# Optimization experiments

Measured on AMD Instinct MI355X. Metric: run time of the kernel, lower is better.

## Reference

```python
import jax, jax.numpy as jnp
import numpy as np


def _rel_shift(x):
    # x: [qlen, klen, bsz, n_head]
    q, k, b, n = x.shape
    zero_pad = jnp.zeros((q, 1, b, n), dtype=x.dtype)
    x_padded = jnp.concatenate([zero_pad, x], axis=1)      # [q, k+1, b, n]
    x_padded = x_padded.reshape(k + 1, q, b, n)            # row-major view
    return x_padded[1:].reshape(q, k, b, n)


def setup_inputs() -> dict:
    key = jax.random.key(0)
    k1, k2, k3, k4, k5 = jax.random.split(key, 5)
    QLEN, KLEN, BSZ, NH, DH = 1024, 1024, 4, 16, 64
    return {
        "w_head_q": jax.random.normal(k1, (QLEN, BSZ, NH, DH), dtype=jnp.float32),
        "w_head_k": jax.random.normal(k2, (KLEN, BSZ, NH, DH), dtype=jnp.float32),
        "r_emb": jax.random.normal(k3, (KLEN, NH, DH), dtype=jnp.float32),
        "r_w_bias": jax.random.normal(k4, (NH, DH), dtype=jnp.float32),
        "r_bias": jax.random.normal(k5, (KLEN, NH), dtype=jnp.float32),
    }


def reference(w_head_q, w_head_k, r_emb, r_w_bias, r_bias):
    klen = w_head_k.shape[0]
    # klen <= r_emb.shape[0] branch: take the last klen relative positions
    r_emb = r_emb[-klen:]
    r_bias = r_bias[-klen:]

    rw_head_q = w_head_q + r_w_bias[None]                  # [q, b, n, d]
    AC = jnp.einsum('ibnd,jbnd->ijbn', rw_head_q, w_head_k)
    B_ = jnp.einsum('ibnd,jnd->ijbn', w_head_q, r_emb)
    D_ = r_bias[None, :, None]                             # [1, k, 1, n]
    BD = _rel_shift(B_ + D_)
    attn_score = AC + BD                                   # [q, k, b, n]
    return attn_score
```

## Files before the change

kernel.cpp:

```cpp
#include <hip/hip_runtime.h>
#include <stdint.h>


typedef __bf16 v8bf __attribute__((ext_vector_type(8)));
typedef float f32x4 __attribute__((ext_vector_type(4)));

union U16x8 { uint4 q; unsigned short us[8]; v8bf v; };

__device__ __forceinline__ unsigned short bf_rne(float f) {
  unsigned int u = __float_as_uint(f);
  return (unsigned short)((u + 0x7fffu + ((u >> 16) & 1u)) >> 16);
}
__device__ __forceinline__ float bf2f(unsigned short h) {
  return __uint_as_float(((unsigned int)h) << 16);
}
__device__ __forceinline__ f32x4 mfma16(v8bf a, v8bf b, f32x4 c) {
  return __builtin_amdgcn_mfma_f32_16x16x32_bf16(a, b, c, 0, 0, 0);
}

template<int N> struct IC { static constexpr int value = N; };

__global__ __launch_bounds__(256) void k_adj(
    const float* __restrict__ r_emb, const float* __restrict__ r_w_bias,
    const float* __restrict__ r_bias, float* __restrict__ adj) {
  int t = blockIdx.x * 256 + threadIdx.x;
  int n = t >> 10, jj = t & 1023;
  const float* re = r_emb + ((size_t)jj * 16 + n) * 64;
  const float* wb = r_w_bias + n * 64;
  float s = 0.f;
#pragma unroll
  for (int d = 0; d < 64; ++d) s += wb[d] * re[d];
  adj[n * 1024 + jj] = r_bias[jj * 16 + n] - s;
}

__global__ __launch_bounds__(256) void k_pack(
    const float* __restrict__ wk, const float* __restrict__ re,
    unsigned short* __restrict__ Kp, unsigned short* __restrict__ Rp) {
  __shared__ float ls[16][68];
  const int gid = blockIdx.x, t = threadIdx.x;
  const int rr = t >> 4, dq = t & 15;
  const float* src;
  unsigned short* dst;
  if (gid < 4096) {
    const int c = gid >> 6, jt = gid & 63, b = c >> 4, n = c & 15;
    src = wk + (size_t)(jt * 16 + rr) * 4096 + b * 1024 + n * 64;
    dst = Kp + (size_t)gid * 2048;
  } else {
    const int g = gid - 4096, n = g >> 6, T = g & 63;
    src = re + ((size_t)(T * 16 + rr) * 16 + n) * 64;
    dst = Rp + (size_t)g * 2048;
  }
  *(float4*)&ls[rr][dq * 4] = *(const float4*)(src + dq * 4);
  __syncthreads();
  const int hl = t >> 7, kc = (t >> 6) & 1, l = t & 63;
  const float* lp = &ls[l & 15][kc * 32 + (l >> 4) * 8];
  U16x8 o;
#pragma unroll
  for (int e = 0; e < 8; ++e) {
    float xe = lp[e];
    unsigned short hi = bf_rne(xe);
    o.us[e] = (hl == 0) ? hi : bf_rne(xe - bf2f(hi));
  }
  *(uint4*)(dst + (size_t)(hl * 2 + kc) * 512 + (size_t)l * 8) = o.q;
}

__global__ __launch_bounds__(512, 2) void k_main(
    const float* __restrict__ q, const float* __restrict__ r_w_bias,
    const unsigned short* __restrict__ Kp_, const unsigned short* __restrict__ Rp_,
    const float* __restrict__ adj, float* __restrict__ out) {
  __shared__ float win[8][32][64];
  __shared__ float outb[8][32][16];
  const int tid = threadIdx.x;
  const int w = tid >> 6, lane = tid & 63;
  const int lr = lane & 15, lh = lane >> 4;
  const int bid = blockIdx.x;
  const int cgrp = bid & 7, iblk = bid >> 3;
  const int i0 = iblk * 32, it0 = iblk * 2, c0 = cgrp * 8;
  const int c = c0 + w, n = c & 15, b = c >> 4;
  const uint4* Kp4 = (const uint4*)Kp_;
  const uint4* Rp4 = (const uint4*)Rp_;

  {
    float4 z = {0.f, 0.f, 0.f, 0.f};
    float4* wp = (float4*)(&win[0][0][0]);
#pragma unroll
    for (int kk = 0; kk < 8; ++kk) wp[tid + kk * 512] = z;
  }

  v8bf Ah[3][2], Al[3][2];
  {
    U16x8 z; z.q = uint4{0u, 0u, 0u, 0u};
#pragma unroll
    for (int itl = 0; itl < 3; ++itl)
#pragma unroll
      for (int kc = 0; kc < 2; ++kc) { Ah[itl][kc] = z.v; Al[itl][kc] = z.v; }
    float wbv[2][8];
#pragma unroll
    for (int kc = 0; kc < 2; ++kc) {
      float4 b0 = *(const float4*)(r_w_bias + n * 64 + kc * 32 + lh * 8);
      float4 b1 = *(const float4*)(r_w_bias + n * 64 + kc * 32 + lh * 8 + 4);
      wbv[kc][0] = b0.x; wbv[kc][1] = b0.y; wbv[kc][2] = b0.z; wbv[kc][3] = b0.w;
      wbv[kc][4] = b1.x; wbv[kc][5] = b1.y; wbv[kc][6] = b1.z; wbv[kc][7] = b1.w;
    }
#pragma unroll
    for (int itl = 0; itl < 3; ++itl) {
      if (it0 + itl <= 63) {
        const float* qp = q + (size_t)(i0 + itl * 16 + lr) * 4096 + b * 1024 + n * 64;
#pragma unroll
        for (int kc = 0; kc < 2; ++kc) {
          float4 xa = *(const float4*)(qp + kc * 32 + lh * 8);
          float4 xb = *(const float4*)(qp + kc * 32 + lh * 8 + 4);
          float x[8] = {xa.x, xa.y, xa.z, xa.w, xb.x, xb.y, xb.z, xb.w};
          U16x8 ph, pl;
#pragma unroll
          for (int e = 0; e < 8; ++e) {
            float xe = x[e] + wbv[kc][e];
            unsigned short hi = bf_rne(xe);
            ph.us[e] = hi;
            pl.us[e] = bf_rne(xe - bf2f(hi));
          }
          Ah[itl][kc] = ph.v; Al[itl][kc] = pl.v;
        }
      }
    }
  }

  v8bf Rh[4][2], Rl[4][2], Kh[2][2], Kl[2][2];

  auto loadR = [&](auto SL, int T) {
    constexpr int S_ = decltype(SL)::value;
#pragma unroll
    for (int hl = 0; hl < 2; ++hl)
#pragma unroll
      for (int kc = 0; kc < 2; ++kc) {
        U16x8 u_;
        u_.q = Rp4[((size_t)(n * 64 + T) * 4 + hl * 2 + kc) * 64 + lane];
        if (hl == 0) Rh[S_][kc] = u_.v; else Rl[S_][kc] = u_.v;
      }
  };
  auto loadK = [&](auto BF, int jt) {
    constexpr int B_ = decltype(BF)::value;
#pragma unroll
    for (int hl = 0; hl < 2; ++hl)
#pragma unroll
      for (int kc = 0; kc < 2; ++kc) {
        U16x8 u_;
        u_.q = Kp4[((size_t)(c * 64 + jt) * 4 + hl * 2 + kc) * 64 + lane];
        if (hl == 0) Kh[B_][kc] = u_.v; else Kl[B_][kc] = u_.v;
      }
  };

  auto body = [&](auto UC, auto PC, int s) {
    constexpr int U = decltype(UC)::value;
    constexpr bool PRO = (decltype(PC)::value != 0);
    if (PRO) loadK(IC<(U + 1) & 1>{}, 0);
    else if (s < 63) loadK(IC<(U + 1) & 1>{}, s + 1);
    loadR(IC<(U + 1) & 3>{}, (s + 1 - it0) & 63);
    float adjv[3];
#pragma unroll
    for (int rt = 0; rt < 3; ++rt) {
      int T = (s - it0 - rt) & 63;
      adjv[rt] = adj[n * 1024 + T * 16 + lr];
    }
    f32x4 acc0 = {0.f, 0.f, 0.f, 0.f}, acc1 = {0.f, 0.f, 0.f, 0.f};
    if (!PRO) {
      constexpr int KB = U & 1;
#pragma unroll
      for (int kc = 0; kc < 2; ++kc) {
        acc0 = mfma16(Ah[0][kc], Kh[KB][kc], acc0);
        acc1 = mfma16(Ah[1][kc], Kh[KB][kc], acc1);
        acc0 = mfma16(Al[0][kc], Kh[KB][kc], acc0);
        acc1 = mfma16(Al[1][kc], Kh[KB][kc], acc1);
        acc0 = mfma16(Ah[0][kc], Kl[KB][kc], acc0);
        acc1 = mfma16(Ah[1][kc], Kl[KB][kc], acc1);
      }
    }
    auto bs = [&](auto RT) {
      constexpr int rt = decltype(RT)::value;
      constexpr int SL = (U - rt + 4) & 3;
      if (it0 + rt > 63) return;
      f32x4 aB = {0.f, 0.f, 0.f, 0.f};
#pragma unroll
      for (int kc = 0; kc < 2; ++kc) {
        aB = mfma16(Ah[rt][kc], Rh[SL][kc], aB);
        aB = mfma16(Al[rt][kc], Rh[SL][kc], aB);
        aB = mfma16(Ah[rt][kc], Rl[SL][kc], aB);
      }
      const int T = (s - it0 - rt) & 63;
      const int vb = T * 16 + lr + i0 + rt * 16 + 4 * lh;
#pragma unroll
      for (int r = 0; r < 4; ++r) {
        int uu = vb + r;
        bool b1 = (uu >= 1023);
        int rowL = rt * 16 + 4 * lh + r - (b1 ? 0 : 1);
        int colS = (uu + 1) & 63;
        float val = aB[r] + adjv[rt];
        bool ok = (rowL >= 0) && (rowL < 32);
        if (PRO) ok = ok && b1;
        if (ok) win[w][rowL][colS] = val;
      }
    };
    bs(IC<0>{}); bs(IC<1>{}); bs(IC<2>{});
    if (PRO) return;
    __syncthreads();
#pragma unroll
    for (int r = 0; r < 4; ++r) {
      outb[w][4 * lh + r][lr] = acc0[r];
      outb[w][16 + 4 * lh + r][lr] = acc1[r];
    }
    {
      constexpr int Z = (U + 3) & 3;
      int row = (tid & 63) >> 1, cc = (tid & 1) * 8;
      float4 z = {0.f, 0.f, 0.f, 0.f};
      *(float4*)&win[w][row][Z * 16 + cc] = z;
      *(float4*)&win[w][row][Z * 16 + cc + 4] = z;
    }
    __syncthreads();
    {
      const int row = tid >> 4, colL = tid & 15;
      const int colS = ((U & 3) * 16) | colL;
      float vv[8];
#pragma unroll
      for (int cl = 0; cl < 8; ++cl)
        vv[cl] = outb[cl][row][colL] + win[cl][row][colS];
      size_t base = ((size_t)(i0 + row) * 1024 + (size_t)(s * 16 + colL)) * 64 + c0;
      float4 o0 = {vv[0], vv[1], vv[2], vv[3]};
      float4 o1 = {vv[4], vv[5], vv[6], vv[7]};
      *(float4*)(out + base) = o0;
      *(float4*)(out + base + 4) = o1;
    }
  };

  loadR(IC<3>{}, (63 - it0) & 63);
  loadR(IC<2>{}, (62 - it0) & 63);
  loadR(IC<1>{}, (61 - it0) & 63);
  __syncthreads();
  body(IC<3>{}, IC<1>{}, -1);
  __syncthreads();

  for (int s4 = 0; s4 < 64; s4 += 4) {
    body(IC<0>{}, IC<0>{}, s4 + 0);
    body(IC<1>{}, IC<0>{}, s4 + 1);
    body(IC<2>{}, IC<0>{}, s4 + 2);
    body(IC<3>{}, IC<0>{}, s4 + 3);
  }
}

extern "C" void kernel_launch(void* const* d_in, const int* in_sizes, int n_in,
                              void* d_out, int out_size, void* d_ws, size_t ws_size,
                              hipStream_t stream) {
  const float* wq  = (const float*)d_in[0];
  const float* wk  = (const float*)d_in[1];
  const float* re  = (const float*)d_in[2];
  const float* rwb = (const float*)d_in[3];
  const float* rb  = (const float*)d_in[4];
  float* out = (float*)d_out;
  char* ws = (char*)d_ws;
  float* adj          = (float*)ws;
  unsigned short* Kp  = (unsigned short*)(ws + 65536);
  unsigned short* Rp  = (unsigned short*)(ws + 65536 + 16777216);
  hipLaunchKernelGGL(k_adj,  dim3(64),   dim3(256), 0, stream, re, rwb, rb, adj);
  hipLaunchKernelGGL(k_pack, dim3(5120), dim3(256), 0, stream, wk, re, Kp, Rp);
  hipLaunchKernelGGL(k_main, dim3(256),  dim3(512), 0, stream, wq, rwb, Kp, Rp, adj, out);
}
```

Measured before the change: 545.3 us.

## Split key range across blocks, swizzle LDS window, use nontemporal output stores

Splits the 64 key tiles into four chunks of 16, launching 1024 blocks instead of 256. Each chunk block runs its own prologue over the preceding tile, so the 256 CUs are better filled. It also XOR-swizzles the LDS window columns to reduce bank conflicts and uses nontemporal stores for the large output. Launch bounds rise to 4 blocks per CU, which may force register spills. Each chunk also repeats some prologue work.

```diff
diff --git a/kernel.cpp b/kernel.cpp
--- a/kernel.cpp
+++ b/kernel.cpp
@@ -16,6 +16,9 @@
 }
 __device__ __forceinline__ f32x4 mfma16(v8bf a, v8bf b, f32x4 c) {
   return __builtin_amdgcn_mfma_f32_16x16x32_bf16(a, b, c, 0, 0, 0);
+}
+__device__ __forceinline__ int wcol(int row, int col) {
+  return col ^ ((row & 3) << 2);
 }
 
 template<int N> struct IC { static constexpr int value = N; };
@@ -64,7 +67,7 @@
   *(uint4*)(dst + (size_t)(hl * 2 + kc) * 512 + (size_t)l * 8) = o.q;
 }
 
-__global__ __launch_bounds__(512, 2) void k_main(
+__global__ __launch_bounds__(512, 4) void k_main(
     const float* __restrict__ q, const float* __restrict__ r_w_bias,
     const unsigned short* __restrict__ Kp_, const unsigned short* __restrict__ Rp_,
     const float* __restrict__ adj, float* __restrict__ out) {
@@ -74,8 +77,10 @@
   const int w = tid >> 6, lane = tid & 63;
   const int lr = lane & 15, lh = lane >> 4;
   const int bid = blockIdx.x;
-  const int cgrp = bid & 7, iblk = bid >> 3;
+  const int cgrp = bid & 7;
+  const int iblk = (bid >> 3) & 31, jc = bid >> 8;
   const int i0 = iblk * 32, it0 = iblk * 2, c0 = cgrp * 8;
+  const int s0 = jc * 16, sEnd = s0 + 16;
   const int c = c0 + w, n = c & 15, b = c >> 4;
   const uint4* Kp4 = (const uint4*)Kp_;
   const uint4* Rp4 = (const uint4*)Rp_;
@@ -152,9 +157,8 @@
 
   auto body = [&](auto UC, auto PC, int s) {
     constexpr int U = decltype(UC)::value;
-    constexpr bool PRO = (decltype(PC)::value != 0);
-    if (PRO) loadK(IC<(U + 1) & 1>{}, 0);
-    else if (s < 63) loadK(IC<(U + 1) & 1>{}, s + 1);
+    constexpr int PRO = decltype(PC)::value;
+    if (PRO || s < sEnd - 1) loadK(IC<(U + 1) & 1>{}, s + 1);
     loadR(IC<(U + 1) & 3>{}, (s + 1 - it0) & 63);
     float adjv[3];
 #pragma unroll
@@ -196,8 +200,8 @@
         int colS = (uu + 1) & 63;
         float val = aB[r] + adjv[rt];
         bool ok = (rowL >= 0) && (rowL < 32);
-        if (PRO) ok = ok && b1;
-        if (ok) win[w][rowL][colS] = val;
+        if (PRO == 1) ok = ok && b1;
+        if (ok) win[w][rowL][wcol(rowL, colS)] = val;
       }
     };
     bs(IC<0>{}); bs(IC<1>{}); bs(IC<2>{});
@@ -212,8 +216,8 @@
       constexpr int Z = (U + 3) & 3;
       int row = (tid & 63) >> 1, cc = (tid & 1) * 8;
       float4 z = {0.f, 0.f, 0.f, 0.f};
-      *(float4*)&win[w][row][Z * 16 + cc] = z;
-      *(float4*)&win[w][row][Z * 16 + cc + 4] = z;
+      *(float4*)&win[w][row][wcol(row, Z * 16 + cc)] = z;
+      *(float4*)&win[w][row][wcol(row, Z * 16 + cc + 4)] = z;
     }
     __syncthreads();
     {
@@ -222,23 +226,24 @@
       float vv[8];
 #pragma unroll
       for (int cl = 0; cl < 8; ++cl)
-        vv[cl] = outb[cl][row][colL] + win[cl][row][colS];
+        vv[cl] = outb[cl][row][colL] + win[cl][row][wcol(row, colS)];
       size_t base = ((size_t)(i0 + row) * 1024 + (size_t)(s * 16 + colL)) * 64 + c0;
-      float4 o0 = {vv[0], vv[1], vv[2], vv[3]};
-      float4 o1 = {vv[4], vv[5], vv[6], vv[7]};
-      *(float4*)(out + base) = o0;
-      *(float4*)(out + base + 4) = o1;
+      f32x4 o0 = {vv[0], vv[1], vv[2], vv[3]};
+      f32x4 o1 = {vv[4], vv[5], vv[6], vv[7]};
+      __builtin_nontemporal_store(o0, (f32x4*)(out + base));
+      __builtin_nontemporal_store(o1, (f32x4*)(out + base + 4));
     }
   };
 
-  loadR(IC<3>{}, (63 - it0) & 63);
-  loadR(IC<2>{}, (62 - it0) & 63);
-  loadR(IC<1>{}, (61 - it0) & 63);
+  loadR(IC<3>{}, (s0 - 1 - it0) & 63);
+  loadR(IC<2>{}, (s0 - 2 - it0) & 63);
+  loadR(IC<1>{}, (s0 - 3 - it0) & 63);
   __syncthreads();
-  body(IC<3>{}, IC<1>{}, -1);
+  if (s0 == 0) body(IC<3>{}, IC<1>{}, -1);
+  else         body(IC<3>{}, IC<2>{}, s0 - 1);
   __syncthreads();
 
-  for (int s4 = 0; s4 < 64; s4 += 4) {
+  for (int s4 = s0; s4 < sEnd; s4 += 4) {
     body(IC<0>{}, IC<0>{}, s4 + 0);
     body(IC<1>{}, IC<0>{}, s4 + 1);
     body(IC<2>{}, IC<0>{}, s4 + 2);
@@ -261,5 +266,5 @@
   unsigned short* Rp  = (unsigned short*)(ws + 65536 + 16777216);
   hipLaunchKernelGGL(k_adj,  dim3(64),   dim3(256), 0, stream, re, rwb, rb, adj);
   hipLaunchKernelGGL(k_pack, dim3(5120), dim3(256), 0, stream, wk, re, Kp, Rp);
-  hipLaunchKernelGGL(k_main, dim3(256),  dim3(512), 0, stream, wq, rwb, Kp, Rp, adj, out);
-}
+  hipLaunchKernelGGL(k_main, dim3(1024), dim3(512), 0, stream, wq, rwb, Kp, Rp, adj, out);
+}
```

Measured after the change: 1.097 ms. +101.2%, slower.
